# Kernel tuning notes

Hardware: AMD Instinct MI355X
Metric: run time of the kernel (lower is better)

## Reference

```python
import jax, jax.numpy as jnp
import numpy as np

T, N = 64, 2048          # timesteps, population
DT = 1e-3                # simulation step
TAU_MEM_INV = 100.0      # LIF membrane 1/tau
V_TH, V_LEAK, V_RESET = 1.0, 0.0, 0.0
TAU_PRE_INV, TAU_POST_INV = 50.0, 50.0   # STDP trace 1/tau
A_PRE, A_POST = 1.0, 1.0                 # trace contributions
ETA_PLUS, ETA_MINUS = 1e-3, 1e-3         # learning rates
W_MIN, W_MAX = 0.0, 1.0                  # hard bounds
ALPHA = 100.0                            # SuperSpike surrogate sharpness

@jax.custom_vjp
def spike(v):
    # Heaviside forward, SuperSpike surrogate backward (as in norse LIF cells)
    return (v > 0.0).astype(v.dtype)

def _spike_fwd(v):
    return spike(v), v

def _spike_bwd(v, g):
    return (g / (ALPHA * jnp.abs(v) + 1.0) ** 2,)

spike.defvjp(_spike_fwd, _spike_bwd)


def setup_inputs() -> dict:
    key = jax.random.key(0)
    k1, k2 = jax.random.split(key)
    # +1.0 bias ensures nonzero spiking activity so STDP actually fires
    exc_current = jax.random.normal(k1, (T, N), dtype=jnp.float32) + 1.0
    # recurrent weights w[post, pre], small positive init within [W_MIN, W_MAX]
    w = jax.random.uniform(k2, (N, N), dtype=jnp.float32) * 0.02
    t_pre = jnp.zeros((N,), jnp.float32)
    t_post = jnp.zeros((N,), jnp.float32)
    return {"exc_current": exc_current, "w": w, "t_pre": t_pre, "t_post": t_post}


def reference(exc_current, w, t_pre, t_post):
    n = w.shape[0]
    z0 = jnp.zeros((n,), w.dtype)  # Layer reset: cell(zeros(population))
    v0 = jnp.zeros((n,), w.dtype)

    def step(carry, x):
        w_, z, v, tp, tpo = carry
        # recurrent synaptic current: w[post, pre] @ z_pre
        i_syn = w_ @ z
        # LIF membrane update
        v = v + DT * TAU_MEM_INV * ((V_LEAK - v) + i_syn + x)
        z_new = spike(v - V_TH)
        v = v * (1.0 - z_new) + V_RESET * z_new  # reset
        # STDP traces (norse stdp_step_linear: update traces, then dw)
        tp = tp + DT * TAU_PRE_INV * (-tp + A_PRE * z_new)
        tpo = tpo + DT * TAU_POST_INV * (-tpo + A_POST * z_new)
        dw = ETA_PLUS * jnp.outer(z_new, tp) - ETA_MINUS * jnp.outer(tpo, z_new)
        w_ = jnp.clip(w_ + dw, W_MIN, W_MAX)  # additive STDP, hard bounds
        return (w_, z_new, v, tp, tpo), z_new

    _, spikes = jax.lax.scan(step, (w, z0, v0, t_pre, t_post), exc_current)
    return spikes  # [T, N], matches torch.stack([self.step(x) for x in exc_current])
```

## Files before the change

kernel.cpp:

```cpp
#include <hip/hip_runtime.h>

constexpr int   T_STEPS = 64;
constexpr int   NN      = 2048;
constexpr float DT_TAU  = 0.1f;
constexpr float V_TH_C  = 1.0f;
constexpr float TRC     = 0.05f;
constexpr float ETA     = 1e-3f;

constexpr int BLOCKS  = 256;
constexpr int THREADS = 512;
constexpr int ROWS_PER_BLOCK = NN / BLOCKS;
constexpr int CHUNKS = NN / 256;

__global__ __launch_bounds__(THREADS)
void snn_msg_kernel(const float* __restrict__ x,
                    const float* __restrict__ w_in,
                    const float* __restrict__ tpre0,
                    const float* __restrict__ tpost0,
                    unsigned long long* __restrict__ zpub,
                    int stride,
                    float*       __restrict__ out)
{
    const int bid  = blockIdx.x;
    const int tid  = threadIdx.x;
    const int wv   = tid >> 6;
    const int lane = tid & 63;
    const int row  = bid * ROWS_PER_BLOCK + wv;

    __shared__ __align__(16) float z_s[NN];
    __shared__ __align__(16) float tp_s[NN];
    __shared__ __align__(16) float x_s[T_STEPS * ROWS_PER_BLOCK];
    __shared__ unsigned word_s[2];

    float4 tpA = make_float4(0.f, 0.f, 0.f, 0.f);
    float4 tpB = tpA;
    if (tid < BLOCKS) {
        tpA = ((const float4*)tpre0)[2 * tid];
        tpB = ((const float4*)tpre0)[2 * tid + 1];
    }

    x_s[tid] = x[(size_t)(tid >> 3) * NN + bid * ROWS_PER_BLOCK + (tid & 7)];

    if (tid < 2) word_s[tid] = 0u;

    float v_own   = 0.0f;
    float tpo_own = tpost0[row];

    const float4* wrow4 = (const float4*)(w_in + (size_t)row * NN);
    float4 wreg[CHUNKS];
    #pragma unroll
    for (int c = 0; c < CHUNKS; ++c) wreg[c] = wrow4[c * 64 + lane];

    const int perm_base = (lane >> 1) + 256 * (lane & 1);

    float isyn = 0.0f;
    float xk   = 0.0f;
    __syncthreads();
    xk = x_s[wv];

    for (int k = 0; k < T_STEPS; ++k) {
        const int par = k & 1;

        float v = v_own + DT_TAU * ((0.0f - v_own) + isyn + xk);
        float z = (v - V_TH_C > 0.0f) ? 1.0f : 0.0f;
        v_own   = v * (1.0f - z);
        tpo_own = tpo_own + TRC * (-tpo_own + z);
        if (lane == 0) {
            out[(size_t)k * NN + row] = z;
            if (k + 1 < T_STEPS) {
                unsigned add = 0x01000000u | (z > 0.0f ? (1u << wv) : 0u);
                unsigned old = __hip_atomic_fetch_add(&word_s[par], add,
                                   __ATOMIC_RELAXED, __HIP_MEMORY_SCOPE_WORKGROUP);
                if ((old >> 24) == 7u) {
                    unsigned bits = (old + add) & 0xFFu;
                    __hip_atomic_store(&word_s[par], 0u,
                                       __ATOMIC_RELAXED, __HIP_MEMORY_SCOPE_WORKGROUP);
                    unsigned long long wrd =
                        ((unsigned long long)(unsigned)(k + 1) << 32) | bits;
                    __hip_atomic_store(&zpub[(size_t)(par * BLOCKS + bid) * stride],
                                       wrd, __ATOMIC_RELAXED,
                                       __HIP_MEMORY_SCOPE_AGENT);
                }
            }
        }
        if (k == T_STEPS - 1) break;

        if (tid < BLOCKS) {
            const unsigned long long* p =
                &zpub[(size_t)(par * BLOCKS + tid) * stride];
            unsigned long long pv = __hip_atomic_load(p, __ATOMIC_RELAXED,
                                        __HIP_MEMORY_SCOPE_AGENT);
            while ((unsigned)(pv >> 32) != (unsigned)(k + 1)) {
                __builtin_amdgcn_s_sleep(1);
                pv = __hip_atomic_load(p, __ATOMIC_RELAXED,
                                       __HIP_MEMORY_SCOPE_AGENT);
            }
            const unsigned bits = (unsigned)pv;
            float4 zA, zB;
            zA.x = (bits & 0x01u) ? 1.0f : 0.0f;
            zA.y = (bits & 0x02u) ? 1.0f : 0.0f;
            zA.z = (bits & 0x04u) ? 1.0f : 0.0f;
            zA.w = (bits & 0x08u) ? 1.0f : 0.0f;
            zB.x = (bits & 0x10u) ? 1.0f : 0.0f;
            zB.y = (bits & 0x20u) ? 1.0f : 0.0f;
            zB.z = (bits & 0x40u) ? 1.0f : 0.0f;
            zB.w = (bits & 0x80u) ? 1.0f : 0.0f;
            tpA.x = tpA.x + TRC * (-tpA.x + zA.x);
            tpA.y = tpA.y + TRC * (-tpA.y + zA.y);
            tpA.z = tpA.z + TRC * (-tpA.z + zA.z);
            tpA.w = tpA.w + TRC * (-tpA.w + zA.w);
            tpB.x = tpB.x + TRC * (-tpB.x + zB.x);
            tpB.y = tpB.y + TRC * (-tpB.y + zB.y);
            tpB.z = tpB.z + TRC * (-tpB.z + zB.z);
            tpB.w = tpB.w + TRC * (-tpB.w + zB.w);
            ((float4*)z_s)[tid]          = zA;
            ((float4*)z_s)[tid + BLOCKS] = zB;
            ((float4*)tp_s)[tid]          = tpA;
            ((float4*)tp_s)[tid + BLOCKS] = tpB;
        }
        __syncthreads();

        const float zi_own = z;
        const float tpoi   = tpo_own;
        xk = x_s[(k + 1) * ROWS_PER_BLOCK + wv];
        float acc = 0.0f;
        const float4* z4s  = (const float4*)z_s;
        const float4* tp4s = (const float4*)tp_s;
        #pragma unroll
        for (int c = 0; c < CHUNKS; ++c) {
            const int slot = c * 32 + perm_base;
            float4 zj = z4s[slot];
            float4 tj = tp4s[slot];
            float nw;
            nw = wreg[c].x + (ETA * (zi_own * tj.x) - ETA * (tpoi * zj.x));
            nw = fminf(fmaxf(nw, 0.0f), 1.0f); wreg[c].x = nw; acc += nw * zj.x;
            nw = wreg[c].y + (ETA * (zi_own * tj.y) - ETA * (tpoi * zj.y));
            nw = fminf(fmaxf(nw, 0.0f), 1.0f); wreg[c].y = nw; acc += nw * zj.y;
            nw = wreg[c].z + (ETA * (zi_own * tj.z) - ETA * (tpoi * zj.z));
            nw = fminf(fmaxf(nw, 0.0f), 1.0f); wreg[c].z = nw; acc += nw * zj.z;
            nw = wreg[c].w + (ETA * (zi_own * tj.w) - ETA * (tpoi * zj.w));
            nw = fminf(fmaxf(nw, 0.0f), 1.0f); wreg[c].w = nw; acc += nw * zj.w;
        }
        #pragma unroll
        for (int m = 32; m >= 1; m >>= 1) acc += __shfl_xor(acc, m, 64);
        isyn = acc;

        __syncthreads();
    }
}

extern "C" void kernel_launch(void* const* d_in, const int* in_sizes, int n_in,
                              void* d_out, int out_size, void* d_ws, size_t ws_size,
                              hipStream_t stream) {
    const float* x     = (const float*)d_in[0];
    const float* w_in  = (const float*)d_in[1];
    const float* tpre  = (const float*)d_in[2];
    const float* tpost = (const float*)d_in[3];
    float*       out   = (float*)d_out;

    unsigned long long* zpub = (unsigned long long*)d_ws;

    int stride;
    if      (ws_size >= (size_t)2 * BLOCKS * 16 * sizeof(unsigned long long)) stride = 16;
    else if (ws_size >= (size_t)2 * BLOCKS *  8 * sizeof(unsigned long long)) stride = 8;
    else                                                                      stride = 1;

    void* args[] = {(void*)&x, (void*)&w_in, (void*)&tpre, (void*)&tpost,
                    (void*)&zpub, (void*)&stride, (void*)&out};
    hipLaunchCooperativeKernel((void*)snn_msg_kernel,
                               dim3(BLOCKS), dim3(THREADS),
                               args, 0, stream);
}
```

Baseline: 262.3 us.

## Double-buffer spike/trace shared arrays, drop trailing barrier, specialize non-spiking rows

Double-buffers the shared z/trace arrays by step parity so the second __syncthreads per step can be removed. Issues the first poll of the cross-block flag before the publish logic, and moves the output store after publishing to shorten the critical path. Adds a fast path for rows that did not spike, which skips the trace loads and the pre-trace term, and switches shared reads to a linear lane layout. Relies on parity buffering being enough to avoid write-after-read races between steps, and the layout change may alter LDS bank behaviour.

Result: slower. 311.0 us (+18.6%).

```diff
diff --git a/kernel.cpp b/kernel.cpp
--- a/kernel.cpp
+++ b/kernel.cpp
@@ -27,8 +27,8 @@
     const int lane = tid & 63;
     const int row  = bid * ROWS_PER_BLOCK + wv;
 
-    __shared__ __align__(16) float z_s[NN];
-    __shared__ __align__(16) float tp_s[NN];
+    __shared__ __align__(16) float z_db[2][NN];
+    __shared__ __align__(16) float tp_db[2][NN];
     __shared__ __align__(16) float x_s[T_STEPS * ROWS_PER_BLOCK];
     __shared__ unsigned word_s[2];
 
@@ -51,8 +51,6 @@
     #pragma unroll
     for (int c = 0; c < CHUNKS; ++c) wreg[c] = wrow4[c * 64 + lane];
 
-    const int perm_base = (lane >> 1) + 256 * (lane & 1);
-
     float isyn = 0.0f;
     float xk   = 0.0f;
     __syncthreads();
@@ -65,8 +63,14 @@
         float z = (v - V_TH_C > 0.0f) ? 1.0f : 0.0f;
         v_own   = v * (1.0f - z);
         tpo_own = tpo_own + TRC * (-tpo_own + z);
+        const unsigned long long* pollp = nullptr;
+        unsigned long long pref = 0;
+        if (tid < BLOCKS && k + 1 < T_STEPS) {
+            pollp = &zpub[(size_t)(par * BLOCKS + tid) * stride];
+            pref = __hip_atomic_load(pollp, __ATOMIC_RELAXED,
+                                     __HIP_MEMORY_SCOPE_AGENT);
+        }
         if (lane == 0) {
-            out[(size_t)k * NN + row] = z;
             if (k + 1 < T_STEPS) {
                 unsigned add = 0x01000000u | (z > 0.0f ? (1u << wv) : 0u);
                 unsigned old = __hip_atomic_fetch_add(&word_s[par], add,
@@ -82,17 +86,15 @@
                                        __HIP_MEMORY_SCOPE_AGENT);
                 }
             }
+            out[(size_t)k * NN + row] = z;
         }
         if (k == T_STEPS - 1) break;
 
         if (tid < BLOCKS) {
-            const unsigned long long* p =
-                &zpub[(size_t)(par * BLOCKS + tid) * stride];
-            unsigned long long pv = __hip_atomic_load(p, __ATOMIC_RELAXED,
-                                        __HIP_MEMORY_SCOPE_AGENT);
+            unsigned long long pv = pref;
             while ((unsigned)(pv >> 32) != (unsigned)(k + 1)) {
                 __builtin_amdgcn_s_sleep(1);
-                pv = __hip_atomic_load(p, __ATOMIC_RELAXED,
+                pv = __hip_atomic_load(pollp, __ATOMIC_RELAXED,
                                        __HIP_MEMORY_SCOPE_AGENT);
             }
             const unsigned bits = (unsigned)pv;
@@ -113,10 +115,10 @@
             tpB.y = tpB.y + TRC * (-tpB.y + zB.y);
             tpB.z = tpB.z + TRC * (-tpB.z + zB.z);
             tpB.w = tpB.w + TRC * (-tpB.w + zB.w);
-            ((float4*)z_s)[tid]          = zA;
-            ((float4*)z_s)[tid + BLOCKS] = zB;
-            ((float4*)tp_s)[tid]          = tpA;
-            ((float4*)tp_s)[tid + BLOCKS] = tpB;
+            ((float4*)z_db[par])[2 * tid]      = zA;
+            ((float4*)z_db[par])[2 * tid + 1]  = zB;
+            ((float4*)tp_db[par])[2 * tid]     = tpA;
+            ((float4*)tp_db[par])[2 * tid + 1] = tpB;
         }
         __syncthreads();
 
@@ -124,28 +126,46 @@
         const float tpoi   = tpo_own;
         xk = x_s[(k + 1) * ROWS_PER_BLOCK + wv];
         float acc = 0.0f;
-        const float4* z4s  = (const float4*)z_s;
-        const float4* tp4s = (const float4*)tp_s;
-        #pragma unroll
-        for (int c = 0; c < CHUNKS; ++c) {
-            const int slot = c * 32 + perm_base;
-            float4 zj = z4s[slot];
-            float4 tj = tp4s[slot];
-            float nw;
-            nw = wreg[c].x + (ETA * (zi_own * tj.x) - ETA * (tpoi * zj.x));
-            nw = fminf(fmaxf(nw, 0.0f), 1.0f); wreg[c].x = nw; acc += nw * zj.x;
-            nw = wreg[c].y + (ETA * (zi_own * tj.y) - ETA * (tpoi * zj.y));
-            nw = fminf(fmaxf(nw, 0.0f), 1.0f); wreg[c].y = nw; acc += nw * zj.y;
-            nw = wreg[c].z + (ETA * (zi_own * tj.z) - ETA * (tpoi * zj.z));
-            nw = fminf(fmaxf(nw, 0.0f), 1.0f); wreg[c].z = nw; acc += nw * zj.z;
-            nw = wreg[c].w + (ETA * (zi_own * tj.w) - ETA * (tpoi * zj.w));
-            nw = fminf(fmaxf(nw, 0.0f), 1.0f); wreg[c].w = nw; acc += nw * zj.w;
+        const float4* z4s  = (const float4*)z_db[par];
+        const float4* tp4s = (const float4*)tp_db[par];
+        if (zi_own != 0.0f) {
+            #pragma unroll
+            for (int c = 0; c < CHUNKS; ++c) {
+                float4 zj = z4s[c * 64 + lane];
+                float4 tj = tp4s[c * 64 + lane];
+                float nw;
+                nw = wreg[c].x + (ETA * (zi_own * tj.x) - ETA * (tpoi * zj.x));
+                nw = fminf(fmaxf(nw, 0.0f), 1.0f); wreg[c].x = nw; acc += nw * zj.x;
+                nw = wreg[c].y + (ETA * (zi_own * tj.y) - ETA * (tpoi * zj.y));
+                nw = fminf(fmaxf(nw, 0.0f), 1.0f); wreg[c].y = nw; acc += nw * zj.y;
+                nw = wreg[c].z + (ETA * (zi_own * tj.z) - ETA * (tpoi * zj.z));
+                nw = fminf(fmaxf(nw, 0.0f), 1.0f); wreg[c].z = nw; acc += nw * zj.z;
+                nw = wreg[c].w + (ETA * (zi_own * tj.w) - ETA * (tpoi * zj.w));
+                nw = fminf(fmaxf(nw, 0.0f), 1.0f); wreg[c].w = nw; acc += nw * zj.w;
+            }
+        } else {
+            const float etp = ETA * tpoi;
+            #pragma unroll
+            for (int c = 0; c < CHUNKS; ++c) {
+                float4 zj = z4s[c * 64 + lane];
+                float nw, nwc;
+                nwc = fminf(fmaxf(wreg[c].x - etp, 0.0f), 1.0f);
+                nw  = (zj.x != 0.0f) ? nwc : wreg[c].x;
+                wreg[c].x = nw; acc += nw * zj.x;
+                nwc = fminf(fmaxf(wreg[c].y - etp, 0.0f), 1.0f);
+                nw  = (zj.y != 0.0f) ? nwc : wreg[c].y;
+                wreg[c].y = nw; acc += nw * zj.y;
+                nwc = fminf(fmaxf(wreg[c].z - etp, 0.0f), 1.0f);
+                nw  = (zj.z != 0.0f) ? nwc : wreg[c].z;
+                wreg[c].z = nw; acc += nw * zj.z;
+                nwc = fminf(fmaxf(wreg[c].w - etp, 0.0f), 1.0f);
+                nw  = (zj.w != 0.0f) ? nwc : wreg[c].w;
+                wreg[c].w = nw; acc += nw * zj.w;
+            }
         }
         #pragma unroll
         for (int m = 32; m >= 1; m >>= 1) acc += __shfl_xor(acc, m, 64);
         isyn = acc;
-
-        __syncthreads();
     }
 }
 
```

## Add push-mode spike exchange where each block writes its word to every consumer

Applied to the files above, without the earlier changes.

Adds a push mode, chosen when the workspace can hold a BLOCKS x BLOCKS mailbox. In this mode each block's 256 threads broadcast its 8-bit spike word into a private slot for every other block. Each consumer then polls only its own slot, so 256 readers no longer poll one shared producer cache line. The cost is 256 scattered remote stores per block per step and a spin-wait in shared memory on the intra-block count.

Result: slower. 364.5 us (+39.0%).

```diff
diff --git a/kernel.cpp b/kernel.cpp
--- a/kernel.cpp
+++ b/kernel.cpp
@@ -19,6 +19,7 @@
                     const float* __restrict__ tpost0,
                     unsigned long long* __restrict__ zpub,
                     int stride,
+                    int push_mode,
                     float*       __restrict__ out)
 {
     const int bid  = blockIdx.x;
@@ -71,7 +72,7 @@
                 unsigned add = 0x01000000u | (z > 0.0f ? (1u << wv) : 0u);
                 unsigned old = __hip_atomic_fetch_add(&word_s[par], add,
                                    __ATOMIC_RELAXED, __HIP_MEMORY_SCOPE_WORKGROUP);
-                if ((old >> 24) == 7u) {
+                if (!push_mode && (old >> 24) == 7u) {
                     unsigned bits = (old + add) & 0xFFu;
                     __hip_atomic_store(&word_s[par], 0u,
                                        __ATOMIC_RELAXED, __HIP_MEMORY_SCOPE_WORKGROUP);
@@ -86,14 +87,37 @@
         if (k == T_STEPS - 1) break;
 
         if (tid < BLOCKS) {
-            const unsigned long long* p =
-                &zpub[(size_t)(par * BLOCKS + tid) * stride];
-            unsigned long long pv = __hip_atomic_load(p, __ATOMIC_RELAXED,
-                                        __HIP_MEMORY_SCOPE_AGENT);
-            while ((unsigned)(pv >> 32) != (unsigned)(k + 1)) {
-                __builtin_amdgcn_s_sleep(1);
+            unsigned long long pv;
+            if (push_mode) {
+                unsigned wrd = __hip_atomic_load(&word_s[par],
+                                   __ATOMIC_RELAXED, __HIP_MEMORY_SCOPE_WORKGROUP);
+                while ((wrd >> 24) != 8u)
+                    wrd = __hip_atomic_load(&word_s[par],
+                              __ATOMIC_RELAXED, __HIP_MEMORY_SCOPE_WORKGROUP);
+                unsigned long long myword =
+                    ((unsigned long long)(unsigned)(k + 1) << 32) | (wrd & 0xFFu);
+                __hip_atomic_store(
+                    &zpub[((size_t)par * BLOCKS + tid) * BLOCKS + bid],
+                    myword, __ATOMIC_RELAXED, __HIP_MEMORY_SCOPE_AGENT);
+                const unsigned long long* p =
+                    &zpub[((size_t)par * BLOCKS + bid) * BLOCKS + tid];
                 pv = __hip_atomic_load(p, __ATOMIC_RELAXED,
                                        __HIP_MEMORY_SCOPE_AGENT);
+                while ((unsigned)(pv >> 32) != (unsigned)(k + 1)) {
+                    __builtin_amdgcn_s_sleep(1);
+                    pv = __hip_atomic_load(p, __ATOMIC_RELAXED,
+                                           __HIP_MEMORY_SCOPE_AGENT);
+                }
+            } else {
+                const unsigned long long* p =
+                    &zpub[(size_t)(par * BLOCKS + tid) * stride];
+                pv = __hip_atomic_load(p, __ATOMIC_RELAXED,
+                                       __HIP_MEMORY_SCOPE_AGENT);
+                while ((unsigned)(pv >> 32) != (unsigned)(k + 1)) {
+                    __builtin_amdgcn_s_sleep(1);
+                    pv = __hip_atomic_load(p, __ATOMIC_RELAXED,
+                                           __HIP_MEMORY_SCOPE_AGENT);
+                }
             }
             const unsigned bits = (unsigned)pv;
             float4 zA, zB;
@@ -120,6 +144,10 @@
         }
         __syncthreads();
 
+        if (push_mode && tid == 0)
+            __hip_atomic_store(&word_s[par], 0u,
+                               __ATOMIC_RELAXED, __HIP_MEMORY_SCOPE_WORKGROUP);
+
         const float zi_own = z;
         const float tpoi   = tpo_own;
         xk = x_s[(k + 1) * ROWS_PER_BLOCK + wv];
@@ -160,13 +188,16 @@
 
     unsigned long long* zpub = (unsigned long long*)d_ws;
 
+    int push_mode =
+        (ws_size >= (size_t)2 * BLOCKS * BLOCKS * sizeof(unsigned long long)) ? 1 : 0;
     int stride;
-    if      (ws_size >= (size_t)2 * BLOCKS * 16 * sizeof(unsigned long long)) stride = 16;
+    if      (push_mode)                                                       stride = 1;
+    else if (ws_size >= (size_t)2 * BLOCKS * 16 * sizeof(unsigned long long)) stride = 16;
     else if (ws_size >= (size_t)2 * BLOCKS *  8 * sizeof(unsigned long long)) stride = 8;
     else                                                                      stride = 1;
 
     void* args[] = {(void*)&x, (void*)&w_in, (void*)&tpre, (void*)&tpost,
-                    (void*)&zpub, (void*)&stride, (void*)&out};
+                    (void*)&zpub, (void*)&stride, (void*)&push_mode, (void*)&out};
     hipLaunchCooperativeKernel((void*)snn_msg_kernel,
                                dim3(BLOCKS), dim3(THREADS),
                                args, 0, stream);
```

## Overlap weight updates with arrival of per-block spike words via chunk flags

Applied to the files above, without the earlier changes.

Replaces the block-wide barrier after polling all spike words with fine-grained per-chunk completion counters in shared memory, so each wave updates its weight chunks as soon as the corresponding 32 spike words have arrived instead of waiting for all 256. The block's own spike word is read from shared memory rather than global, which removes one agent-scope round trip. The dot product is deferred to after all chunks are processed. This adds polling loops in every wave, dynamic switch dispatch on register arrays (which risks spilling or indexing overhead), and more shared-memory atomics.

After: 478.5 us. 82.4% more time.

```diff
diff --git a/kernel.cpp b/kernel.cpp
--- a/kernel.cpp
+++ b/kernel.cpp
@@ -31,6 +31,8 @@
     __shared__ __align__(16) float tp_s[NN];
     __shared__ __align__(16) float x_s[T_STEPS * ROWS_PER_BLOCK];
     __shared__ unsigned word_s[2];
+    __shared__ unsigned long long ownword_s[2];
+    __shared__ unsigned done4_s[2];
 
     float4 tpA = make_float4(0.f, 0.f, 0.f, 0.f);
     float4 tpB = tpA;
@@ -41,7 +43,7 @@
 
     x_s[tid] = x[(size_t)(tid >> 3) * NN + bid * ROWS_PER_BLOCK + (tid & 7)];
 
-    if (tid < 2) word_s[tid] = 0u;
+    if (tid < 2) { word_s[tid] = 0u; done4_s[tid] = 0u; }
 
     float v_own   = 0.0f;
     float tpo_own = tpost0[row];
@@ -52,11 +54,65 @@
     for (int c = 0; c < CHUNKS; ++c) wreg[c] = wrow4[c * 64 + lane];
 
     const int perm_base = (lane >> 1) + 256 * (lane & 1);
+    const bool ownlocal = (tid == bid);
 
     float isyn = 0.0f;
     float xk   = 0.0f;
     __syncthreads();
     xk = x_s[wv];
+
+    const float4* z4s  = (const float4*)z_s;
+    const float4* tp4s = (const float4*)tp_s;
+
+#define PROC_CHUNK(c_)                                                         \
+    {                                                                          \
+        const int slot = (c_) * 32 + perm_base;                                \
+        float4 zj = z4s[slot];                                                 \
+        float4 tj = tp4s[slot];                                                \
+        float nw;                                                              \
+        nw = wreg[c_].x + (ETA * (zi_own * tj.x) - ETA * (tpoi * zj.x));       \
+        nw = fminf(fmaxf(nw, 0.0f), 1.0f); wreg[c_].x = nw;                    \
+        nw = wreg[c_].y + (ETA * (zi_own * tj.y) - ETA * (tpoi * zj.y));       \
+        nw = fminf(fmaxf(nw, 0.0f), 1.0f); wreg[c_].y = nw;                    \
+        nw = wreg[c_].z + (ETA * (zi_own * tj.z) - ETA * (tpoi * zj.z));       \
+        nw = fminf(fmaxf(nw, 0.0f), 1.0f); wreg[c_].z = nw;                    \
+        nw = wreg[c_].w + (ETA * (zi_own * tj.w) - ETA * (tpoi * zj.w));       \
+        nw = fminf(fmaxf(nw, 0.0f), 1.0f); wreg[c_].w = nw;                    \
+        zst[c_] = zj;                                                          \
+    }
+
+#define TRY_CONSUME()                                                          \
+    {                                                                          \
+        unsigned d0 = __hip_atomic_load(&done4_s[0], __ATOMIC_ACQUIRE,         \
+                                        __HIP_MEMORY_SCOPE_WORKGROUP);         \
+        unsigned d1 = __hip_atomic_load(&done4_s[1], __ATOMIC_ACQUIRE,         \
+                                        __HIP_MEMORY_SCOPE_WORKGROUP);         \
+        unsigned rm = 0;                                                       \
+        rm |= (((d0 >>  0) & 0xFFu) == tag8) ? 0x01u : 0u;                     \
+        rm |= (((d0 >>  8) & 0xFFu) == tag8) ? 0x02u : 0u;                     \
+        rm |= (((d0 >> 16) & 0xFFu) == tag8) ? 0x04u : 0u;                     \
+        rm |= (((d0 >> 24) & 0xFFu) == tag8) ? 0x08u : 0u;                     \
+        rm |= (((d1 >>  0) & 0xFFu) == tag8) ? 0x10u : 0u;                     \
+        rm |= (((d1 >>  8) & 0xFFu) == tag8) ? 0x20u : 0u;                     \
+        rm |= (((d1 >> 16) & 0xFFu) == tag8) ? 0x40u : 0u;                     \
+        rm |= (((d1 >> 24) & 0xFFu) == tag8) ? 0x80u : 0u;                     \
+        rm &= ~(unsigned)processed;                                            \
+        if (rm) {                                                              \
+            int c_ = (int)__builtin_ctz(rm);                                   \
+            switch (c_) {                                                      \
+            case 0: PROC_CHUNK(0); break;                                      \
+            case 1: PROC_CHUNK(1); break;                                      \
+            case 2: PROC_CHUNK(2); break;                                      \
+            case 3: PROC_CHUNK(3); break;                                      \
+            case 4: PROC_CHUNK(4); break;                                      \
+            case 5: PROC_CHUNK(5); break;                                      \
+            case 6: PROC_CHUNK(6); break;                                      \
+            default: PROC_CHUNK(7); break;                                     \
+            }                                                                  \
+            processed |= 1 << c_;                                              \
+            did = true;                                                        \
+        }                                                                      \
+    }
 
     for (int k = 0; k < T_STEPS; ++k) {
         const int par = k & 1;
@@ -77,6 +133,8 @@
                                        __ATOMIC_RELAXED, __HIP_MEMORY_SCOPE_WORKGROUP);
                     unsigned long long wrd =
                         ((unsigned long long)(unsigned)(k + 1) << 32) | bits;
+                    __hip_atomic_store(&ownword_s[par], wrd,
+                                       __ATOMIC_RELAXED, __HIP_MEMORY_SCOPE_WORKGROUP);
                     __hip_atomic_store(&zpub[(size_t)(par * BLOCKS + bid) * stride],
                                        wrd, __ATOMIC_RELAXED,
                                        __HIP_MEMORY_SCOPE_AGENT);
@@ -85,68 +143,105 @@
         }
         if (k == T_STEPS - 1) break;
 
-        if (tid < BLOCKS) {
-            const unsigned long long* p =
+        const float    zi_own = z;
+        const float    tpoi   = tpo_own;
+        const unsigned tag    = (unsigned)(k + 1);
+        const unsigned tag8   = (unsigned)(k + 1);
+        float4 zst[CHUNKS];
+        int processed = 0;
+
+        if (wv < 4) {
+            const unsigned long long* pollp =
                 &zpub[(size_t)(par * BLOCKS + tid) * stride];
-            unsigned long long pv = __hip_atomic_load(p, __ATOMIC_RELAXED,
-                                        __HIP_MEMORY_SCOPE_AGENT);
-            while ((unsigned)(pv >> 32) != (unsigned)(k + 1)) {
-                __builtin_amdgcn_s_sleep(1);
-                pv = __hip_atomic_load(p, __ATOMIC_RELAXED,
-                                       __HIP_MEMORY_SCOPE_AGENT);
+            bool mypend = true;
+            bool flagLo = false, flagHi = false;
+            while (processed != 0xFF || __ballot(mypend)) {
+                bool did = false;
+                unsigned long long pmask = __ballot(mypend);
+                unsigned long long pv = 0;
+                if (pmask && mypend) {
+                    pv = ownlocal
+                       ? __hip_atomic_load(&ownword_s[par], __ATOMIC_RELAXED,
+                                           __HIP_MEMORY_SCOPE_WORKGROUP)
+                       : __hip_atomic_load(pollp, __ATOMIC_RELAXED,
+                                           __HIP_MEMORY_SCOPE_AGENT);
+                }
+                TRY_CONSUME();
+                if (pmask) {
+                    bool newready = mypend && ((unsigned)(pv >> 32) == tag);
+                    if (newready) {
+                        const unsigned bits = (unsigned)pv;
+                        float4 zA, zB;
+                        zA.x = (bits & 0x01u) ? 1.0f : 0.0f;
+                        zA.y = (bits & 0x02u) ? 1.0f : 0.0f;
+                        zA.z = (bits & 0x04u) ? 1.0f : 0.0f;
+                        zA.w = (bits & 0x08u) ? 1.0f : 0.0f;
+                        zB.x = (bits & 0x10u) ? 1.0f : 0.0f;
+                        zB.y = (bits & 0x20u) ? 1.0f : 0.0f;
+                        zB.z = (bits & 0x40u) ? 1.0f : 0.0f;
+                        zB.w = (bits & 0x80u) ? 1.0f : 0.0f;
+                        tpA.x = tpA.x + TRC * (-tpA.x + zA.x);
+                        tpA.y = tpA.y + TRC * (-tpA.y + zA.y);
+                        tpA.z = tpA.z + TRC * (-tpA.z + zA.z);
+                        tpA.w = tpA.w + TRC * (-tpA.w + zA.w);
+                        tpB.x = tpB.x + TRC * (-tpB.x + zB.x);
+                        tpB.y = tpB.y + TRC * (-tpB.y + zB.y);
+                        tpB.z = tpB.z + TRC * (-tpB.z + zB.z);
+                        tpB.w = tpB.w + TRC * (-tpB.w + zB.w);
+                        ((float4*)z_s)[tid]           = zA;
+                        ((float4*)z_s)[tid + BLOCKS]  = zB;
+                        ((float4*)tp_s)[tid]          = tpA;
+                        ((float4*)tp_s)[tid + BLOCKS] = tpB;
+                        mypend = false;
+                        did = true;
+                    }
+                    unsigned long long pm2 = __ballot(mypend);
+                    if (!flagLo && (pm2 & 0xFFFFFFFFull) == 0ull) {
+                        if (lane == 0) {
+                            const int cc = 2 * wv;
+                            __hip_atomic_fetch_add(&done4_s[cc >> 2],
+                                1u << (8 * (cc & 3)),
+                                __ATOMIC_RELEASE, __HIP_MEMORY_SCOPE_WORKGROUP);
+                        }
+                        flagLo = true;
+                    }
+                    if (!flagHi && (pm2 >> 32) == 0ull) {
+                        if (lane == 0) {
+                            const int cc = 2 * wv + 1;
+                            __hip_atomic_fetch_add(&done4_s[cc >> 2],
+                                1u << (8 * (cc & 3)),
+                                __ATOMIC_RELEASE, __HIP_MEMORY_SCOPE_WORKGROUP);
+                        }
+                        flagHi = true;
+                    }
+                }
+                if (!did) __builtin_amdgcn_s_sleep(1);
             }
-            const unsigned bits = (unsigned)pv;
-            float4 zA, zB;
-            zA.x = (bits & 0x01u) ? 1.0f : 0.0f;
-            zA.y = (bits & 0x02u) ? 1.0f : 0.0f;
-            zA.z = (bits & 0x04u) ? 1.0f : 0.0f;
-            zA.w = (bits & 0x08u) ? 1.0f : 0.0f;
-            zB.x = (bits & 0x10u) ? 1.0f : 0.0f;
-            zB.y = (bits & 0x20u) ? 1.0f : 0.0f;
-            zB.z = (bits & 0x40u) ? 1.0f : 0.0f;
-            zB.w = (bits & 0x80u) ? 1.0f : 0.0f;
-            tpA.x = tpA.x + TRC * (-tpA.x + zA.x);
-            tpA.y = tpA.y + TRC * (-tpA.y + zA.y);
-            tpA.z = tpA.z + TRC * (-tpA.z + zA.z);
-            tpA.w = tpA.w + TRC * (-tpA.w + zA.w);
-            tpB.x = tpB.x + TRC * (-tpB.x + zB.x);
-            tpB.y = tpB.y + TRC * (-tpB.y + zB.y);
-            tpB.z = tpB.z + TRC * (-tpB.z + zB.z);
-            tpB.w = tpB.w + TRC * (-tpB.w + zB.w);
-            ((float4*)z_s)[tid]          = zA;
-            ((float4*)z_s)[tid + BLOCKS] = zB;
-            ((float4*)tp_s)[tid]          = tpA;
-            ((float4*)tp_s)[tid + BLOCKS] = tpB;
+        } else {
+            while (processed != 0xFF) {
+                bool did = false;
+                TRY_CONSUME();
+                if (!did) __builtin_amdgcn_s_sleep(1);
+            }
         }
-        __syncthreads();
-
-        const float zi_own = z;
-        const float tpoi   = tpo_own;
-        xk = x_s[(k + 1) * ROWS_PER_BLOCK + wv];
+
         float acc = 0.0f;
-        const float4* z4s  = (const float4*)z_s;
-        const float4* tp4s = (const float4*)tp_s;
         #pragma unroll
         for (int c = 0; c < CHUNKS; ++c) {
-            const int slot = c * 32 + perm_base;
-            float4 zj = z4s[slot];
-            float4 tj = tp4s[slot];
-            float nw;
-            nw = wreg[c].x + (ETA * (zi_own * tj.x) - ETA * (tpoi * zj.x));
-            nw = fminf(fmaxf(nw, 0.0f), 1.0f); wreg[c].x = nw; acc += nw * zj.x;
-            nw = wreg[c].y + (ETA * (zi_own * tj.y) - ETA * (tpoi * zj.y));
-            nw = fminf(fmaxf(nw, 0.0f), 1.0f); wreg[c].y = nw; acc += nw * zj.y;
-            nw = wreg[c].z + (ETA * (zi_own * tj.z) - ETA * (tpoi * zj.z));
-            nw = fminf(fmaxf(nw, 0.0f), 1.0f); wreg[c].z = nw; acc += nw * zj.z;
-            nw = wreg[c].w + (ETA * (zi_own * tj.w) - ETA * (tpoi * zj.w));
-            nw = fminf(fmaxf(nw, 0.0f), 1.0f); wreg[c].w = nw; acc += nw * zj.w;
+            acc += wreg[c].x * zst[c].x;
+            acc += wreg[c].y * zst[c].y;
+            acc += wreg[c].z * zst[c].z;
+            acc += wreg[c].w * zst[c].w;
         }
         #pragma unroll
         for (int m = 32; m >= 1; m >>= 1) acc += __shfl_xor(acc, m, 64);
         isyn = acc;
+        xk = x_s[(k + 1) * ROWS_PER_BLOCK + wv];
 
         __syncthreads();
     }
+#undef TRY_CONSUME
+#undef PROC_CHUNK
 }
 
 extern "C" void kernel_launch(void* const* d_in, const int* in_sizes, int n_in,
```
